# Optimization experiments

Hardware: AMD Instinct MI355X
Metric: run time of the kernel (lower is better)

## Reference

```python
import jax, jax.numpy as jnp
import numpy as np

N, E, ND, ED, NG = 100000, 1600000, 256, 32, 64
H1, H2 = 5, 1  # hard-coded hidden widths in the module
EPS = 1e-5


def setup_inputs() -> dict:
    key = jax.random.key(0)
    ks = jax.random.split(key, 32)

    def rn(k, shape, scale=0.05):
        return jax.random.normal(k, shape, dtype=jnp.float32) * scale

    inp = {
        "x": rn(ks[0], (N, ND), 1.0),
        "edge_attr": rn(ks[1], (E, ED), 1.0),
        "edge_index": jax.random.randint(ks[2], (2, E), 0, N, dtype=jnp.int32),
        "batch_idx": jnp.sort(jax.random.randint(ks[3], (N,), 0, NG, dtype=jnp.int32)),
        # conv1: ResGatedGraphConv(ND -> H1) with edge_dim=ED, root_weight, bias
        "Wk1": rn(ks[4], (ND, H1)), "bk1": jnp.zeros((H1,), jnp.float32),
        "Wq1": rn(ks[5], (ND, H1)), "bq1": jnp.zeros((H1,), jnp.float32),
        "Wv1": rn(ks[6], (ND, H1)), "bv1": jnp.zeros((H1,), jnp.float32),
        "We1": rn(ks[7], (ED, H1)), "be1": jnp.zeros((H1,), jnp.float32),
        "Ws1": rn(ks[8], (ND, H1)), "b1": jnp.zeros((H1,), jnp.float32),
        # GraphNorm(H1): weight=1, bias=0, mean_scale=1 at init
        "gw": jnp.ones((H1,), jnp.float32), "gb": jnp.zeros((H1,), jnp.float32),
        "gms": jnp.ones((H1,), jnp.float32),
        # conv2: ResGatedGraphConv(H1 -> H2)
        "Wk2": rn(ks[9], (H1, H2)), "bk2": jnp.zeros((H2,), jnp.float32),
        "Wq2": rn(ks[10], (H1, H2)), "bq2": jnp.zeros((H2,), jnp.float32),
        "Wv2": rn(ks[11], (H1, H2)), "bv2": jnp.zeros((H2,), jnp.float32),
        "We2": rn(ks[12], (ED, H2)), "be2": jnp.zeros((H2,), jnp.float32),
        "Ws2": rn(ks[13], (H1, H2)), "b2": jnp.zeros((H2,), jnp.float32),
    }
    return inp


def _res_gated_conv(x, src, dst, eatt, Wk, bk, Wq, bq, Wv, bv, We, be, Ws, b):
    # PyG ResGatedGraphConv: msg = sigmoid(k_i + q_j) * v_j with edge_attr
    # projection added to k, q, v; aggr='add'; plus root skip and bias.
    k = x @ Wk + bk            # [N,H]
    q = x @ Wq + bq            # [N,H]
    v = x @ Wv + bv            # [N,H]
    e = eatt @ We + be         # [E,H]
    gate = jax.nn.sigmoid(k[dst] + q[src] + 2.0 * e)  # (k_i+e)+(q_j+e)
    msg = gate * (v[src] + e)                          # [E,H]
    agg = jax.ops.segment_sum(msg, dst, num_segments=x.shape[0])
    return agg + x @ Ws + b


def _graph_norm(x, batch, w, b, ms):
    ones = jnp.ones((x.shape[0], 1), x.dtype)
    cnt = jnp.maximum(jax.ops.segment_sum(ones, batch, num_segments=NG), 1.0)
    mean = jax.ops.segment_sum(x, batch, num_segments=NG) / cnt
    out = x - mean[batch] * ms
    var = jax.ops.segment_sum(out * out, batch, num_segments=NG) / cnt
    inv_std = jax.lax.rsqrt(var + EPS)
    return w * out * inv_std[batch] + b


def reference(x, edge_attr, edge_index, batch_idx,
              Wk1, bk1, Wq1, bq1, Wv1, bv1, We1, be1, Ws1, b1,
              gw, gb, gms,
              Wk2, bk2, Wq2, bq2, Wv2, bv2, We2, be2, Ws2, b2):
    src, dst = edge_index[0], edge_index[1]
    h = _res_gated_conv(x, src, dst, edge_attr, Wk1, bk1, Wq1, bq1, Wv1, bv1,
                        We1, be1, Ws1, b1)
    h = _graph_norm(h, batch_idx, gw, gb, gms)
    h = jax.nn.relu(h)
    h = _res_gated_conv(h, src, dst, edge_attr, Wk2, bk2, Wq2, bq2, Wv2, bv2,
                        We2, be2, Ws2, b2)
    return jax.nn.sigmoid(h)
```

## Files before the change

### kernel.cpp

```cpp
#include <hip/hip_runtime.h>
#include <math.h>

#define ND 256
#define ED 32
#define H1 5
#define NG 64
#define SCAN_TILE 1024

__device__ __forceinline__ float sigf(float z) {
    return 1.0f / (1.0f + __expf(-z));
}

__global__ void node_proj1(const float* __restrict__ x,
                           const float* __restrict__ Wk, const float* __restrict__ bk,
                           const float* __restrict__ Wq, const float* __restrict__ bq,
                           const float* __restrict__ Wv, const float* __restrict__ bv,
                           const float* __restrict__ Ws, const float* __restrict__ br,
                           float* __restrict__ kqv, float* __restrict__ h, int N)
{
    int n = blockIdx.x * blockDim.x + threadIdx.x;
    if (n >= N) return;

    float acc[20];
#pragma unroll
    for (int c = 0; c < H1; c++) {
        acc[c]      = bk[c];
        acc[5 + c]  = bq[c];
        acc[10 + c] = bv[c];
        acc[15 + c] = br[c];
    }

    const float4* X4 = (const float4*)(x + (size_t)n * ND);
#pragma unroll 2
    for (int j4 = 0; j4 < ND / 4; j4++) {
        float4 xv = X4[j4];
        float xr[4] = {xv.x, xv.y, xv.z, xv.w};
#pragma unroll
        for (int r = 0; r < 4; r++) {
            int j = j4 * 4 + r;
#pragma unroll
            for (int c = 0; c < H1; c++) {
                acc[c]      += xr[r] * Wk[j * H1 + c];
                acc[5 + c]  += xr[r] * Wq[j * H1 + c];
                acc[10 + c] += xr[r] * Wv[j * H1 + c];
                acc[15 + c] += xr[r] * Ws[j * H1 + c];
            }
        }
    }

    float* row = kqv + (size_t)n * 16;
#pragma unroll
    for (int c = 0; c < H1; c++) {
        row[c]      = acc[5 + c];
        row[5 + c]  = acc[10 + c];
        row[10 + c] = acc[c];
    }
    row[15] = 0.0f;
#pragma unroll
    for (int c = 0; c < H1; c++) h[(size_t)n * H1 + c] = acc[15 + c];
}

__global__ void hist_dst(const int* __restrict__ ei, int* __restrict__ cnt, int E)
{
    int e = blockIdx.x * blockDim.x + threadIdx.x;
    if (e < E) atomicAdd(&cnt[ei[E + e]], 1);
}

__global__ void scan_part(const int* __restrict__ cnt, int* __restrict__ bsum, int N)
{
    int t = threadIdx.x;
    int base = blockIdx.x * SCAN_TILE + t * 4;
    int s = 0;
    if (base + 3 < N) {
        int4 v = *(const int4*)(cnt + base);
        s = v.x + v.y + v.z + v.w;
    } else {
        for (int i = 0; i < 4; i++) if (base + i < N) s += cnt[base + i];
    }
#pragma unroll
    for (int off = 32; off >= 1; off >>= 1) s += __shfl_xor(s, off);
    __shared__ int wsum[4];
    if ((t & 63) == 0) wsum[t >> 6] = s;
    __syncthreads();
    if (t == 0) bsum[blockIdx.x] = wsum[0] + wsum[1] + wsum[2] + wsum[3];
}

__global__ void scan_blocksums(int* __restrict__ bsum, int nb)
{
    __shared__ int a[1024], b[1024];
    int t = threadIdx.x;
    int v = (t < nb) ? bsum[t] : 0;
    a[t] = v;
    __syncthreads();
    int* in = a; int* out = b;
    for (int off = 1; off < 1024; off <<= 1) {
        out[t] = in[t] + ((t >= off) ? in[t - off] : 0);
        __syncthreads();
        int* tmp = in; in = out; out = tmp;
    }
    if (t < nb) bsum[t] = in[t] - v;
}

__global__ void scan_final(const int* __restrict__ cnt, const int* __restrict__ bsum,
                           int* __restrict__ offs, int* __restrict__ cursor, int N, int E)
{
    int t = threadIdx.x;
    int lane = t & 63;
    int wave = t >> 6;
    int base = blockIdx.x * SCAN_TILE + t * 4;

    int v0 = 0, v1 = 0, v2 = 0, v3 = 0;
    if (base + 3 < N) {
        int4 v = *(const int4*)(cnt + base);
        v0 = v.x; v1 = v.y; v2 = v.z; v3 = v.w;
    } else {
        if (base + 0 < N) v0 = cnt[base + 0];
        if (base + 1 < N) v1 = cnt[base + 1];
        if (base + 2 < N) v2 = cnt[base + 2];
        if (base + 3 < N) v3 = cnt[base + 3];
    }
    int s = v0 + v1 + v2 + v3;

    int inc = s;
#pragma unroll
    for (int off = 1; off < 64; off <<= 1) {
        int u = __shfl_up(inc, off);
        if (lane >= off) inc += u;
    }

    __shared__ int wtot[4];
    if (lane == 63) wtot[wave] = inc;
    __syncthreads();
    int woff = 0;
#pragma unroll
    for (int w = 0; w < 4; w++) woff += (w < wave) ? wtot[w] : 0;

    int excl = bsum[blockIdx.x] + woff + (inc - s);

    if (base < N) {
        int p0 = excl, p1 = p0 + v0, p2 = p1 + v1, p3 = p2 + v2;
        if (base + 3 < N) {
            *(int4*)(offs + base)   = make_int4(p0, p1, p2, p3);
            *(int4*)(cursor + base) = make_int4(p0, p1, p2, p3);
        } else {
            if (base + 0 < N) { offs[base + 0] = p0; cursor[base + 0] = p0; }
            if (base + 1 < N) { offs[base + 1] = p1; cursor[base + 1] = p1; }
            if (base + 2 < N) { offs[base + 2] = p2; cursor[base + 2] = p2; }
            if (base + 3 < N) { offs[base + 3] = p3; cursor[base + 3] = p3; }
        }
    }
    if (blockIdx.x == 0 && t == 0) offs[N] = E;
}

__global__ void edge_scatter(const float* __restrict__ ea, const int* __restrict__ ei,
                             const float* __restrict__ We1, const float* __restrict__ be1,
                             const float* __restrict__ We2, const float* __restrict__ be2,
                             int* __restrict__ cursor, float* __restrict__ sorted, int E)
{
    __shared__ float lds[256 * 33];
    int t = threadIdx.x;
    int base = blockIdx.x * 256;
    int nEdge = min(256, E - base);

    const float4* g = (const float4*)(ea + (size_t)base * ED);
    for (int k = t; k < nEdge * 8; k += 256) {
        float4 v = g[k];
        int f = k * 4;
        int r = f >> 5, c = f & 31;
        float* p = &lds[r * 33 + c];
        p[0] = v.x; p[1] = v.y; p[2] = v.z; p[3] = v.w;
    }
    __syncthreads();

    int e = base + t;
    if (e >= E) return;

    float acc0 = be1[0], acc1 = be1[1], acc2 = be1[2], acc3 = be1[3], acc4 = be1[4];
    float acc5 = be2[0];
    const float* myrow = &lds[t * 33];
#pragma unroll
    for (int j = 0; j < ED; j++) {
        float a = myrow[j];
        acc0 += a * We1[j * H1 + 0];
        acc1 += a * We1[j * H1 + 1];
        acc2 += a * We1[j * H1 + 2];
        acc3 += a * We1[j * H1 + 3];
        acc4 += a * We1[j * H1 + 4];
        acc5 += a * We2[j];
    }

    int s = ei[e];
    int d = ei[E + e];
    int pos = atomicAdd(&cursor[d], 1);

    float4* rec = (float4*)(sorted + (size_t)pos * 8);
    rec[0] = make_float4(__int_as_float(s), acc0, acc1, acc2);
    rec[1] = make_float4(acc3, acc4, acc5, 0.0f);
}

__global__ void aggregate1(const float* __restrict__ sorted, const int* __restrict__ offs,
                           const float* __restrict__ kqv, float* __restrict__ h, int N)
{
    int t = threadIdx.x;
    int n = blockIdx.x * 16 + (t >> 4);
    int lane = t & 15;
    if (n >= N) return;

    int start = offs[n], end = offs[n + 1];

    const float4* row = (const float4*)(kqv + (size_t)n * 16);
    float4 kA = row[2];
    float4 kB = row[3];
    float kd0 = kA.z, kd1 = kA.w, kd2 = kB.x, kd3 = kB.y, kd4 = kB.z;

    float m0 = 0, m1 = 0, m2 = 0, m3 = 0, m4 = 0;
    for (int i = start + lane; i < end; i += 16) {
        const float4* rec = (const float4*)(sorted + (size_t)i * 8);
        float4 r0 = rec[0];
        float4 r1 = rec[1];
        int s = __float_as_int(r0.x);
        const float4* srow = (const float4*)(kqv + (size_t)s * 16);
        float4 q0 = srow[0];
        float4 q1 = srow[1];
        float4 q2 = srow[2];
        m0 += sigf(kd0 + q0.x + 2.0f * r0.y) * (q1.y + r0.y);
        m1 += sigf(kd1 + q0.y + 2.0f * r0.z) * (q1.z + r0.z);
        m2 += sigf(kd2 + q0.z + 2.0f * r0.w) * (q1.w + r0.w);
        m3 += sigf(kd3 + q0.w + 2.0f * r1.x) * (q2.x + r1.x);
        m4 += sigf(kd4 + q1.x + 2.0f * r1.y) * (q2.y + r1.y);
    }

#pragma unroll
    for (int off = 8; off >= 1; off >>= 1) {
        m0 += __shfl_xor(m0, off);
        m1 += __shfl_xor(m1, off);
        m2 += __shfl_xor(m2, off);
        m3 += __shfl_xor(m3, off);
        m4 += __shfl_xor(m4, off);
    }

    if (lane == 0) {
        size_t base = (size_t)n * H1;
        h[base + 0] += m0;
        h[base + 1] += m1;
        h[base + 2] += m2;
        h[base + 3] += m3;
        h[base + 4] += m4;
    }
}

__global__ void norm_reduce(const float* __restrict__ h, const int* __restrict__ B,
                            const float* __restrict__ gw, const float* __restrict__ gb,
                            const float* __restrict__ gms,
                            float* __restrict__ scale, float* __restrict__ shift, int N)
{
    int g = blockIdx.x;

    int lo = 0, hi = N;
    while (lo < hi) { int mid = (lo + hi) >> 1; if (B[mid] < g) lo = mid + 1; else hi = mid; }
    int start = lo;
    hi = N;
    while (lo < hi) { int mid = (lo + hi) >> 1; if (B[mid] < g + 1) lo = mid + 1; else hi = mid; }
    int end = lo;

    float sum[H1] = {0, 0, 0, 0, 0};
    float sq[H1]  = {0, 0, 0, 0, 0};
    for (int i = start + threadIdx.x; i < end; i += blockDim.x) {
#pragma unroll
        for (int c = 0; c < H1; c++) {
            float v = h[(size_t)i * H1 + c];
            sum[c] += v;
            sq[c]  += v * v;
        }
    }

#pragma unroll
    for (int off = 32; off >= 1; off >>= 1) {
#pragma unroll
        for (int c = 0; c < H1; c++) {
            sum[c] += __shfl_xor(sum[c], off);
            sq[c]  += __shfl_xor(sq[c], off);
        }
    }

    __shared__ float ls[4][2 * H1];
    int wave = threadIdx.x >> 6;
    int lane = threadIdx.x & 63;
    if (lane == 0) {
#pragma unroll
        for (int c = 0; c < H1; c++) { ls[wave][c] = sum[c]; ls[wave][H1 + c] = sq[c]; }
    }
    __syncthreads();

    if (threadIdx.x == 0) {
        float cnt = fmaxf((float)(end - start), 1.0f);
#pragma unroll
        for (int c = 0; c < H1; c++) {
            float s0 = ls[0][c] + ls[1][c] + ls[2][c] + ls[3][c];
            float q0 = ls[0][H1 + c] + ls[1][H1 + c] + ls[2][H1 + c] + ls[3][H1 + c];
            float mean = s0 / cnt;
            float ms   = gms[c];
            float var  = q0 / cnt - mean * mean * ms * (2.0f - ms);
            float inv  = rsqrtf(var + 1e-5f);
            float sc   = gw[c] * inv;
            scale[g * H1 + c] = sc;
            shift[g * H1 + c] = gb[c] - sc * mean * ms;
        }
    }
}

__global__ void norm_apply_proj2(const float* __restrict__ h, const int* __restrict__ B,
                                 const float* __restrict__ scale, const float* __restrict__ shift,
                                 const float* __restrict__ Wk2, const float* __restrict__ bk2,
                                 const float* __restrict__ Wq2, const float* __restrict__ bq2,
                                 const float* __restrict__ Wv2, const float* __restrict__ bv2,
                                 const float* __restrict__ Ws2, const float* __restrict__ b2,
                                 float4* __restrict__ kqv2, float* __restrict__ root2, int N)
{
    int n = blockIdx.x * blockDim.x + threadIdx.x;
    if (n >= N) return;

    int g = B[n];
    float k2 = bk2[0], q2 = bq2[0], v2 = bv2[0], s2 = b2[0];
#pragma unroll
    for (int c = 0; c < H1; c++) {
        float hn = scale[g * H1 + c] * h[(size_t)n * H1 + c] + shift[g * H1 + c];
        hn = fmaxf(hn, 0.0f);
        k2 += hn * Wk2[c];
        q2 += hn * Wq2[c];
        v2 += hn * Wv2[c];
        s2 += hn * Ws2[c];
    }
    kqv2[n]  = make_float4(k2, q2, v2, 0.0f);
    root2[n] = s2;
}

__global__ void aggregate2(const float* __restrict__ sorted, const int* __restrict__ offs,
                           const float4* __restrict__ kqv2, const float* __restrict__ root2,
                           float* __restrict__ out, int N)
{
    int t = threadIdx.x;
    int n = blockIdx.x * 16 + (t >> 4);
    int lane = t & 15;
    if (n >= N) return;

    int start = offs[n], end = offs[n + 1];
    float kd = kqv2[n].x;

    float m = 0;
    for (int i = start + lane; i < end; i += 16) {
        const float4* rec = (const float4*)(sorted + (size_t)i * 8);
        float4 r0 = rec[0];
        float4 r1 = rec[1];
        int s = __float_as_int(r0.x);
        float e2 = r1.z;
        float4 sv = kqv2[s];
        m += sigf(kd + sv.y + 2.0f * e2) * (sv.z + e2);
    }

#pragma unroll
    for (int off = 8; off >= 1; off >>= 1) m += __shfl_xor(m, off);

    if (lane == 0) out[n] = sigf(root2[n] + m);
}

extern "C" void kernel_launch(void* const* d_in, const int* in_sizes, int n_in,
                              void* d_out, int out_size, void* d_ws, size_t ws_size,
                              hipStream_t stream)
{
    const float* x   = (const float*)d_in[0];
    const float* ea  = (const float*)d_in[1];
    const int*   ei  = (const int*)d_in[2];
    const int*   B   = (const int*)d_in[3];
    const float* Wk1 = (const float*)d_in[4];
    const float* bk1 = (const float*)d_in[5];
    const float* Wq1 = (const float*)d_in[6];
    const float* bq1 = (const float*)d_in[7];
    const float* Wv1 = (const float*)d_in[8];
    const float* bv1 = (const float*)d_in[9];
    const float* We1 = (const float*)d_in[10];
    const float* be1 = (const float*)d_in[11];
    const float* Ws1 = (const float*)d_in[12];
    const float* b1  = (const float*)d_in[13];
    const float* gw  = (const float*)d_in[14];
    const float* gb  = (const float*)d_in[15];
    const float* gms = (const float*)d_in[16];
    const float* Wk2 = (const float*)d_in[17];
    const float* bk2 = (const float*)d_in[18];
    const float* Wq2 = (const float*)d_in[19];
    const float* bq2 = (const float*)d_in[20];
    const float* Wv2 = (const float*)d_in[21];
    const float* bv2 = (const float*)d_in[22];
    const float* We2 = (const float*)d_in[23];
    const float* be2 = (const float*)d_in[24];
    const float* Ws2 = (const float*)d_in[25];
    const float* b2  = (const float*)d_in[26];

    const int N = in_sizes[0] / ND;
    const int E = in_sizes[1] / ED;
    const int nb = (N + SCAN_TILE - 1) / SCAN_TILE;

    float* ws      = (float*)d_ws;
    float* kqv     = ws;
    float* h       = kqv + (size_t)N * 16;
    float* sorted  = h + (size_t)N * H1;
    int*   cnt     = (int*)(sorted + (size_t)E * 8);
    int*   offs    = cnt + N;
    int*   cursor  = offs + N + 4;
    int*   bsum    = cursor + N;
    float* scale   = (float*)(bsum + 1024);
    float* shift   = scale + NG * H1;
    float* kqv2f   = shift + NG * H1 + 2;
    kqv2f = (float*)(bsum + 1024) + 640;
    float* root2   = kqv2f + (size_t)N * 4;
    float4* kqv2   = (float4*)kqv2f;

    dim3 blk(256);
    dim3 gN((N + 255) / 256);
    dim3 gE((E + 255) / 256);
    dim3 gAgg((N + 15) / 16);

    hipMemsetAsync(cnt, 0, (size_t)N * sizeof(int), stream);

    hist_dst<<<gE, blk, 0, stream>>>(ei, cnt, E);
    node_proj1<<<gN, blk, 0, stream>>>(x, Wk1, bk1, Wq1, bq1, Wv1, bv1, Ws1, b1,
                                       kqv, h, N);
    scan_part<<<nb, 256, 0, stream>>>(cnt, bsum, N);
    scan_blocksums<<<1, 1024, 0, stream>>>(bsum, nb);
    scan_final<<<nb, 256, 0, stream>>>(cnt, bsum, offs, cursor, N, E);
    edge_scatter<<<gE, blk, 0, stream>>>(ea, ei, We1, be1, We2, be2, cursor, sorted, E);
    aggregate1<<<gAgg, blk, 0, stream>>>(sorted, offs, kqv, h, N);
    norm_reduce<<<NG, blk, 0, stream>>>(h, B, gw, gb, gms, scale, shift, N);
    norm_apply_proj2<<<gN, blk, 0, stream>>>(h, B, scale, shift,
                                             Wk2, bk2, Wq2, bq2, Wv2, bv2, Ws2, b2,
                                             kqv2, root2, N);
    aggregate2<<<gAgg, blk, 0, stream>>>(sorted, offs, kqv2, root2, (float*)d_out, N);
}
```

Before: 654.0 us.

## Replace CSR sort-and-gather aggregation with per-edge atomic scatter

Removes the histogram, three-pass scan and counting-sort scatter that built a destination-sorted edge list. Each edge now computes its projection, message and gate directly and atomically adds into the destination node's accumulators for both conv layers. A small per-edge buffer keeps the layer-2 edge projection. This drops several kernel launches and the sorted record traffic, but it makes float atomics contend on destinations and makes the summation order nondeterministic. Loading edge_attr per thread as float4 rows also gives up the coalesced LDS staging the old scatter kernel used.

```diff
diff --git a/kernel.cpp b/kernel.cpp
--- a/kernel.cpp
+++ b/kernel.cpp
@@ -5,7 +5,6 @@
 #define ED 32
 #define H1 5
 #define NG 64
-#define SCAN_TILE 1024
 
 __device__ __forceinline__ float sigf(float z) {
     return 1.0f / (1.0f + __expf(-z));
@@ -60,193 +59,63 @@
     for (int c = 0; c < H1; c++) h[(size_t)n * H1 + c] = acc[15 + c];
 }
 
-__global__ void hist_dst(const int* __restrict__ ei, int* __restrict__ cnt, int E)
+__global__ void edge1(const float* __restrict__ ea, const int* __restrict__ ei,
+                      const float* __restrict__ We1, const float* __restrict__ be1,
+                      const float* __restrict__ We2, const float* __restrict__ be2,
+                      const float* __restrict__ kqv, float* __restrict__ h,
+                      float* __restrict__ e2buf, int E)
 {
     int e = blockIdx.x * blockDim.x + threadIdx.x;
-    if (e < E) atomicAdd(&cnt[ei[E + e]], 1);
-}
-
-__global__ void scan_part(const int* __restrict__ cnt, int* __restrict__ bsum, int N)
-{
-    int t = threadIdx.x;
-    int base = blockIdx.x * SCAN_TILE + t * 4;
-    int s = 0;
-    if (base + 3 < N) {
-        int4 v = *(const int4*)(cnt + base);
-        s = v.x + v.y + v.z + v.w;
-    } else {
-        for (int i = 0; i < 4; i++) if (base + i < N) s += cnt[base + i];
-    }
-#pragma unroll
-    for (int off = 32; off >= 1; off >>= 1) s += __shfl_xor(s, off);
-    __shared__ int wsum[4];
-    if ((t & 63) == 0) wsum[t >> 6] = s;
-    __syncthreads();
-    if (t == 0) bsum[blockIdx.x] = wsum[0] + wsum[1] + wsum[2] + wsum[3];
-}
-
-__global__ void scan_blocksums(int* __restrict__ bsum, int nb)
-{
-    __shared__ int a[1024], b[1024];
-    int t = threadIdx.x;
-    int v = (t < nb) ? bsum[t] : 0;
-    a[t] = v;
-    __syncthreads();
-    int* in = a; int* out = b;
-    for (int off = 1; off < 1024; off <<= 1) {
-        out[t] = in[t] + ((t >= off) ? in[t - off] : 0);
-        __syncthreads();
-        int* tmp = in; in = out; out = tmp;
-    }
-    if (t < nb) bsum[t] = in[t] - v;
-}
-
-__global__ void scan_final(const int* __restrict__ cnt, const int* __restrict__ bsum,
-                           int* __restrict__ offs, int* __restrict__ cursor, int N, int E)
-{
-    int t = threadIdx.x;
-    int lane = t & 63;
-    int wave = t >> 6;
-    int base = blockIdx.x * SCAN_TILE + t * 4;
-
-    int v0 = 0, v1 = 0, v2 = 0, v3 = 0;
-    if (base + 3 < N) {
-        int4 v = *(const int4*)(cnt + base);
-        v0 = v.x; v1 = v.y; v2 = v.z; v3 = v.w;
-    } else {
-        if (base + 0 < N) v0 = cnt[base + 0];
-        if (base + 1 < N) v1 = cnt[base + 1];
-        if (base + 2 < N) v2 = cnt[base + 2];
-        if (base + 3 < N) v3 = cnt[base + 3];
-    }
-    int s = v0 + v1 + v2 + v3;
-
-    int inc = s;
-#pragma unroll
-    for (int off = 1; off < 64; off <<= 1) {
-        int u = __shfl_up(inc, off);
-        if (lane >= off) inc += u;
-    }
-
-    __shared__ int wtot[4];
-    if (lane == 63) wtot[wave] = inc;
-    __syncthreads();
-    int woff = 0;
-#pragma unroll
-    for (int w = 0; w < 4; w++) woff += (w < wave) ? wtot[w] : 0;
-
-    int excl = bsum[blockIdx.x] + woff + (inc - s);
-
-    if (base < N) {
-        int p0 = excl, p1 = p0 + v0, p2 = p1 + v1, p3 = p2 + v2;
-        if (base + 3 < N) {
-            *(int4*)(offs + base)   = make_int4(p0, p1, p2, p3);
-            *(int4*)(cursor + base) = make_int4(p0, p1, p2, p3);
-        } else {
-            if (base + 0 < N) { offs[base + 0] = p0; cursor[base + 0] = p0; }
-            if (base + 1 < N) { offs[base + 1] = p1; cursor[base + 1] = p1; }
-            if (base + 2 < N) { offs[base + 2] = p2; cursor[base + 2] = p2; }
-            if (base + 3 < N) { offs[base + 3] = p3; cursor[base + 3] = p3; }
-        }
-    }
-    if (blockIdx.x == 0 && t == 0) offs[N] = E;
-}
-
-__global__ void edge_scatter(const float* __restrict__ ea, const int* __restrict__ ei,
-                             const float* __restrict__ We1, const float* __restrict__ be1,
-                             const float* __restrict__ We2, const float* __restrict__ be2,
-                             int* __restrict__ cursor, float* __restrict__ sorted, int E)
-{
-    __shared__ float lds[256 * 33];
-    int t = threadIdx.x;
-    int base = blockIdx.x * 256;
-    int nEdge = min(256, E - base);
-
-    const float4* g = (const float4*)(ea + (size_t)base * ED);
-    for (int k = t; k < nEdge * 8; k += 256) {
-        float4 v = g[k];
-        int f = k * 4;
-        int r = f >> 5, c = f & 31;
-        float* p = &lds[r * 33 + c];
-        p[0] = v.x; p[1] = v.y; p[2] = v.z; p[3] = v.w;
-    }
-    __syncthreads();
-
-    int e = base + t;
     if (e >= E) return;
 
-    float acc0 = be1[0], acc1 = be1[1], acc2 = be1[2], acc3 = be1[3], acc4 = be1[4];
-    float acc5 = be2[0];
-    const float* myrow = &lds[t * 33];
-#pragma unroll
-    for (int j = 0; j < ED; j++) {
-        float a = myrow[j];
-        acc0 += a * We1[j * H1 + 0];
-        acc1 += a * We1[j * H1 + 1];
-        acc2 += a * We1[j * H1 + 2];
-        acc3 += a * We1[j * H1 + 3];
-        acc4 += a * We1[j * H1 + 4];
-        acc5 += a * We2[j];
-    }
+    const float4* A4 = (const float4*)(ea + (size_t)e * ED);
+    float4 r[8];
+#pragma unroll
+    for (int j = 0; j < 8; j++) r[j] = A4[j];
 
     int s = ei[e];
     int d = ei[E + e];
-    int pos = atomicAdd(&cursor[d], 1);
-
-    float4* rec = (float4*)(sorted + (size_t)pos * 8);
-    rec[0] = make_float4(__int_as_float(s), acc0, acc1, acc2);
-    rec[1] = make_float4(acc3, acc4, acc5, 0.0f);
-}
-
-__global__ void aggregate1(const float* __restrict__ sorted, const int* __restrict__ offs,
-                           const float* __restrict__ kqv, float* __restrict__ h, int N)
-{
-    int t = threadIdx.x;
-    int n = blockIdx.x * 16 + (t >> 4);
-    int lane = t & 15;
-    if (n >= N) return;
-
-    int start = offs[n], end = offs[n + 1];
-
-    const float4* row = (const float4*)(kqv + (size_t)n * 16);
-    float4 kA = row[2];
-    float4 kB = row[3];
-    float kd0 = kA.z, kd1 = kA.w, kd2 = kB.x, kd3 = kB.y, kd4 = kB.z;
-
-    float m0 = 0, m1 = 0, m2 = 0, m3 = 0, m4 = 0;
-    for (int i = start + lane; i < end; i += 16) {
-        const float4* rec = (const float4*)(sorted + (size_t)i * 8);
-        float4 r0 = rec[0];
-        float4 r1 = rec[1];
-        int s = __float_as_int(r0.x);
-        const float4* srow = (const float4*)(kqv + (size_t)s * 16);
-        float4 q0 = srow[0];
-        float4 q1 = srow[1];
-        float4 q2 = srow[2];
-        m0 += sigf(kd0 + q0.x + 2.0f * r0.y) * (q1.y + r0.y);
-        m1 += sigf(kd1 + q0.y + 2.0f * r0.z) * (q1.z + r0.z);
-        m2 += sigf(kd2 + q0.z + 2.0f * r0.w) * (q1.w + r0.w);
-        m3 += sigf(kd3 + q0.w + 2.0f * r1.x) * (q2.x + r1.x);
-        m4 += sigf(kd4 + q1.x + 2.0f * r1.y) * (q2.y + r1.y);
-    }
-
-#pragma unroll
-    for (int off = 8; off >= 1; off >>= 1) {
-        m0 += __shfl_xor(m0, off);
-        m1 += __shfl_xor(m1, off);
-        m2 += __shfl_xor(m2, off);
-        m3 += __shfl_xor(m3, off);
-        m4 += __shfl_xor(m4, off);
-    }
-
-    if (lane == 0) {
-        size_t base = (size_t)n * H1;
-        h[base + 0] += m0;
-        h[base + 1] += m1;
-        h[base + 2] += m2;
-        h[base + 3] += m3;
-        h[base + 4] += m4;
-    }
+
+    float e10 = be1[0], e11 = be1[1], e12 = be1[2], e13 = be1[3], e14 = be1[4];
+    float e2  = be2[0];
+#pragma unroll
+    for (int j4 = 0; j4 < 8; j4++) {
+        float av[4] = {r[j4].x, r[j4].y, r[j4].z, r[j4].w};
+#pragma unroll
+        for (int t = 0; t < 4; t++) {
+            int j = j4 * 4 + t;
+            float a = av[t];
+            e10 += a * We1[j * H1 + 0];
+            e11 += a * We1[j * H1 + 1];
+            e12 += a * We1[j * H1 + 2];
+            e13 += a * We1[j * H1 + 3];
+            e14 += a * We1[j * H1 + 4];
+            e2  += a * We2[j];
+        }
+    }
+
+    const float4* srow = (const float4*)(kqv + (size_t)s * 16);
+    float4 q0 = srow[0];
+    float4 q1 = srow[1];
+    float4 q2 = srow[2];
+    const float4* drow = (const float4*)(kqv + (size_t)d * 16);
+    float4 kA = drow[2];
+    float4 kB = drow[3];
+
+    float m0 = sigf(kA.z + q0.x + 2.0f * e10) * (q1.y + e10);
+    float m1 = sigf(kA.w + q0.y + 2.0f * e11) * (q1.z + e11);
+    float m2 = sigf(kB.x + q0.z + 2.0f * e12) * (q1.w + e12);
+    float m3 = sigf(kB.y + q0.w + 2.0f * e13) * (q2.x + e13);
+    float m4 = sigf(kB.z + q1.x + 2.0f * e14) * (q2.y + e14);
+
+    float* hd = h + (size_t)d * H1;
+    atomicAdd(hd + 0, m0);
+    atomicAdd(hd + 1, m1);
+    atomicAdd(hd + 2, m2);
+    atomicAdd(hd + 3, m3);
+    atomicAdd(hd + 4, m4);
+
+    e2buf[e] = e2;
 }
 
 __global__ void norm_reduce(const float* __restrict__ h, const int* __restrict__ B,
@@ -335,33 +204,26 @@
     root2[n] = s2;
 }
 
-__global__ void aggregate2(const float* __restrict__ sorted, const int* __restrict__ offs,
-                           const float4* __restrict__ kqv2, const float* __restrict__ root2,
-                           float* __restrict__ out, int N)
-{
-    int t = threadIdx.x;
-    int n = blockIdx.x * 16 + (t >> 4);
-    int lane = t & 15;
-    if (n >= N) return;
-
-    int start = offs[n], end = offs[n + 1];
-    float kd = kqv2[n].x;
-
-    float m = 0;
-    for (int i = start + lane; i < end; i += 16) {
-        const float4* rec = (const float4*)(sorted + (size_t)i * 8);
-        float4 r0 = rec[0];
-        float4 r1 = rec[1];
-        int s = __float_as_int(r0.x);
-        float e2 = r1.z;
-        float4 sv = kqv2[s];
-        m += sigf(kd + sv.y + 2.0f * e2) * (sv.z + e2);
-    }
-
-#pragma unroll
-    for (int off = 8; off >= 1; off >>= 1) m += __shfl_xor(m, off);
-
-    if (lane == 0) out[n] = sigf(root2[n] + m);
+__global__ void edge2(const int* __restrict__ ei, const float* __restrict__ e2buf,
+                      const float4* __restrict__ kqv2, float* __restrict__ mbuf, int E)
+{
+    int e = blockIdx.x * blockDim.x + threadIdx.x;
+    if (e >= E) return;
+
+    int s = ei[e];
+    int d = ei[E + e];
+    float e2 = e2buf[e];
+    float4 sv = kqv2[s];
+    float kd = kqv2[d].x;
+    float m = sigf(kd + sv.y + 2.0f * e2) * (sv.z + e2);
+    atomicAdd(&mbuf[d], m);
+}
+
+__global__ void finalize(const float* __restrict__ root2, const float* __restrict__ mbuf,
+                         float* __restrict__ out, int N)
+{
+    int n = blockIdx.x * blockDim.x + threadIdx.x;
+    if (n < N) out[n] = sigf(root2[n] + mbuf[n]);
 }
 
 extern "C" void kernel_launch(void* const* d_in, const int* in_sizes, int n_in,
@@ -398,41 +260,31 @@
 
     const int N = in_sizes[0] / ND;
     const int E = in_sizes[1] / ED;
-    const int nb = (N + SCAN_TILE - 1) / SCAN_TILE;
-
-    float* ws      = (float*)d_ws;
-    float* kqv     = ws;
-    float* h       = kqv + (size_t)N * 16;
-    float* sorted  = h + (size_t)N * H1;
-    int*   cnt     = (int*)(sorted + (size_t)E * 8);
-    int*   offs    = cnt + N;
-    int*   cursor  = offs + N + 4;
-    int*   bsum    = cursor + N;
-    float* scale   = (float*)(bsum + 1024);
-    float* shift   = scale + NG * H1;
-    float* kqv2f   = shift + NG * H1 + 2;
-    kqv2f = (float*)(bsum + 1024) + 640;
-    float* root2   = kqv2f + (size_t)N * 4;
-    float4* kqv2   = (float4*)kqv2f;
+
+    float* ws     = (float*)d_ws;
+    float* kqv    = ws;
+    float* h      = kqv + (size_t)N * 16;
+    float* e2buf  = h + (size_t)N * H1;
+    float* scale  = e2buf + (size_t)E;
+    float* shift  = scale + NG * H1;
+    float* kqv2f  = shift + NG * H1;
+    float* root2  = kqv2f + (size_t)N * 4;
+    float* mbuf   = root2 + (size_t)N;
+    float4* kqv2  = (float4*)kqv2f;
 
     dim3 blk(256);
     dim3 gN((N + 255) / 256);
     dim3 gE((E + 255) / 256);
-    dim3 gAgg((N + 15) / 16);
-
-    hipMemsetAsync(cnt, 0, (size_t)N * sizeof(int), stream);
-
-    hist_dst<<<gE, blk, 0, stream>>>(ei, cnt, E);
+
+    hipMemsetAsync(mbuf, 0, (size_t)N * sizeof(float), stream);
+
     node_proj1<<<gN, blk, 0, stream>>>(x, Wk1, bk1, Wq1, bq1, Wv1, bv1, Ws1, b1,
                                        kqv, h, N);
-    scan_part<<<nb, 256, 0, stream>>>(cnt, bsum, N);
-    scan_blocksums<<<1, 1024, 0, stream>>>(bsum, nb);
-    scan_final<<<nb, 256, 0, stream>>>(cnt, bsum, offs, cursor, N, E);
-    edge_scatter<<<gE, blk, 0, stream>>>(ea, ei, We1, be1, We2, be2, cursor, sorted, E);
-    aggregate1<<<gAgg, blk, 0, stream>>>(sorted, offs, kqv, h, N);
+    edge1<<<gE, blk, 0, stream>>>(ea, ei, We1, be1, We2, be2, kqv, h, e2buf, E);
     norm_reduce<<<NG, blk, 0, stream>>>(h, B, gw, gb, gms, scale, shift, N);
     norm_apply_proj2<<<gN, blk, 0, stream>>>(h, B, scale, shift,
                                              Wk2, bk2, Wq2, bq2, Wv2, bv2, Ws2, b2,
                                              kqv2, root2, N);
-    aggregate2<<<gAgg, blk, 0, stream>>>(sorted, offs, kqv2, root2, (float*)d_out, N);
-}
+    edge2<<<gE, blk, 0, stream>>>(ei, e2buf, kqv2, mbuf, E);
+    finalize<<<gN, blk, 0, stream>>>(root2, mbuf, (float*)d_out, N);
+}
```

After: 917.3 us. 1.4x slower.

## Compute layer-1 edge messages in edge order and aggregate through a permutation index

Applied to the files above, without the earlier changes.

The edge kernel now reads the k/q/v rows of source and destination and computes the full layer-1 message per edge, writing it coherently at the edge's own index. A permutation array maps CSR slots to edge ids. aggregate1 then only sums precomputed messages via the permutation, and aggregate2 gathers the edge term and the source index through it. The scattered 32-byte record writes become coalesced writes, and the gather work moves from aggregation into the edge kernel. In exchange the aggregation reads become indirect, edge_msg reads the edge attributes per thread without the LDS staging it used before, and aggregate2 now does an extra indirect read of edge_index.

```diff
diff --git a/kernel.cpp b/kernel.cpp
--- a/kernel.cpp
+++ b/kernel.cpp
@@ -152,54 +152,66 @@
     if (blockIdx.x == 0 && t == 0) offs[N] = E;
 }
 
-__global__ void edge_scatter(const float* __restrict__ ea, const int* __restrict__ ei,
-                             const float* __restrict__ We1, const float* __restrict__ be1,
-                             const float* __restrict__ We2, const float* __restrict__ be2,
-                             int* __restrict__ cursor, float* __restrict__ sorted, int E)
-{
-    __shared__ float lds[256 * 33];
-    int t = threadIdx.x;
-    int base = blockIdx.x * 256;
-    int nEdge = min(256, E - base);
-
-    const float4* g = (const float4*)(ea + (size_t)base * ED);
-    for (int k = t; k < nEdge * 8; k += 256) {
-        float4 v = g[k];
-        int f = k * 4;
-        int r = f >> 5, c = f & 31;
-        float* p = &lds[r * 33 + c];
-        p[0] = v.x; p[1] = v.y; p[2] = v.z; p[3] = v.w;
-    }
-    __syncthreads();
-
-    int e = base + t;
+__global__ void edge_msg(const float* __restrict__ ea, const int* __restrict__ ei,
+                         const float* __restrict__ We1, const float* __restrict__ be1,
+                         const float* __restrict__ We2, const float* __restrict__ be2,
+                         const float* __restrict__ kqv, int* __restrict__ cursor,
+                         float4* __restrict__ recA, float2* __restrict__ recB,
+                         int* __restrict__ perm, int E)
+{
+    int e = blockIdx.x * blockDim.x + threadIdx.x;
     if (e >= E) return;
 
-    float acc0 = be1[0], acc1 = be1[1], acc2 = be1[2], acc3 = be1[3], acc4 = be1[4];
-    float acc5 = be2[0];
-    const float* myrow = &lds[t * 33];
-#pragma unroll
-    for (int j = 0; j < ED; j++) {
-        float a = myrow[j];
-        acc0 += a * We1[j * H1 + 0];
-        acc1 += a * We1[j * H1 + 1];
-        acc2 += a * We1[j * H1 + 2];
-        acc3 += a * We1[j * H1 + 3];
-        acc4 += a * We1[j * H1 + 4];
-        acc5 += a * We2[j];
-    }
+    const float4* A4 = (const float4*)(ea + (size_t)e * ED);
+    float4 r[8];
+#pragma unroll
+    for (int j = 0; j < 8; j++) r[j] = A4[j];
 
     int s = ei[e];
     int d = ei[E + e];
     int pos = atomicAdd(&cursor[d], 1);
 
-    float4* rec = (float4*)(sorted + (size_t)pos * 8);
-    rec[0] = make_float4(__int_as_float(s), acc0, acc1, acc2);
-    rec[1] = make_float4(acc3, acc4, acc5, 0.0f);
-}
-
-__global__ void aggregate1(const float* __restrict__ sorted, const int* __restrict__ offs,
-                           const float* __restrict__ kqv, float* __restrict__ h, int N)
+    const float4* srow = (const float4*)(kqv + (size_t)s * 16);
+    float4 q0 = srow[0];
+    float4 q1 = srow[1];
+    float4 q2 = srow[2];
+    const float4* drow = (const float4*)(kqv + (size_t)d * 16);
+    float4 kA = drow[2];
+    float4 kB = drow[3];
+
+    float e10 = be1[0], e11 = be1[1], e12 = be1[2], e13 = be1[3], e14 = be1[4];
+    float e2  = be2[0];
+#pragma unroll
+    for (int j4 = 0; j4 < 8; j4++) {
+        float av[4] = {r[j4].x, r[j4].y, r[j4].z, r[j4].w};
+#pragma unroll
+        for (int t = 0; t < 4; t++) {
+            int j = j4 * 4 + t;
+            float a = av[t];
+            e10 += a * We1[j * H1 + 0];
+            e11 += a * We1[j * H1 + 1];
+            e12 += a * We1[j * H1 + 2];
+            e13 += a * We1[j * H1 + 3];
+            e14 += a * We1[j * H1 + 4];
+            e2  += a * We2[j];
+        }
+    }
+
+    float m0 = sigf(kA.z + q0.x + 2.0f * e10) * (q1.y + e10);
+    float m1 = sigf(kA.w + q0.y + 2.0f * e11) * (q1.z + e11);
+    float m2 = sigf(kB.x + q0.z + 2.0f * e12) * (q1.w + e12);
+    float m3 = sigf(kB.y + q0.w + 2.0f * e13) * (q2.x + e13);
+    float m4 = sigf(kB.z + q1.x + 2.0f * e14) * (q2.y + e14);
+
+    recA[e] = make_float4(m0, m1, m2, m3);
+    recB[e] = make_float2(m4, e2);
+
+    perm[pos] = e;
+}
+
+__global__ void aggregate1(const int* __restrict__ perm, const int* __restrict__ offs,
+                           const float4* __restrict__ recA, const float2* __restrict__ recB,
+                           float* __restrict__ h, int N)
 {
     int t = threadIdx.x;
     int n = blockIdx.x * 16 + (t >> 4);
@@ -208,26 +220,12 @@
 
     int start = offs[n], end = offs[n + 1];
 
-    const float4* row = (const float4*)(kqv + (size_t)n * 16);
-    float4 kA = row[2];
-    float4 kB = row[3];
-    float kd0 = kA.z, kd1 = kA.w, kd2 = kB.x, kd3 = kB.y, kd4 = kB.z;
-
     float m0 = 0, m1 = 0, m2 = 0, m3 = 0, m4 = 0;
     for (int i = start + lane; i < end; i += 16) {
-        const float4* rec = (const float4*)(sorted + (size_t)i * 8);
-        float4 r0 = rec[0];
-        float4 r1 = rec[1];
-        int s = __float_as_int(r0.x);
-        const float4* srow = (const float4*)(kqv + (size_t)s * 16);
-        float4 q0 = srow[0];
-        float4 q1 = srow[1];
-        float4 q2 = srow[2];
-        m0 += sigf(kd0 + q0.x + 2.0f * r0.y) * (q1.y + r0.y);
-        m1 += sigf(kd1 + q0.y + 2.0f * r0.z) * (q1.z + r0.z);
-        m2 += sigf(kd2 + q0.z + 2.0f * r0.w) * (q1.w + r0.w);
-        m3 += sigf(kd3 + q0.w + 2.0f * r1.x) * (q2.x + r1.x);
-        m4 += sigf(kd4 + q1.x + 2.0f * r1.y) * (q2.y + r1.y);
+        int e = perm[i];
+        float4 a = recA[e];
+        float2 b = recB[e];
+        m0 += a.x; m1 += a.y; m2 += a.z; m3 += a.w; m4 += b.x;
     }
 
 #pragma unroll
@@ -335,7 +333,8 @@
     root2[n] = s2;
 }
 
-__global__ void aggregate2(const float* __restrict__ sorted, const int* __restrict__ offs,
+__global__ void aggregate2(const int* __restrict__ perm, const int* __restrict__ offs,
+                           const float2* __restrict__ recB, const int* __restrict__ ei,
                            const float4* __restrict__ kqv2, const float* __restrict__ root2,
                            float* __restrict__ out, int N)
 {
@@ -349,11 +348,10 @@
 
     float m = 0;
     for (int i = start + lane; i < end; i += 16) {
-        const float4* rec = (const float4*)(sorted + (size_t)i * 8);
-        float4 r0 = rec[0];
-        float4 r1 = rec[1];
-        int s = __float_as_int(r0.x);
-        float e2 = r1.z;
+        int e = perm[i];
+        float2 b = recB[e];
+        float e2 = b.y;
+        int s = ei[e];
         float4 sv = kqv2[s];
         m += sigf(kd + sv.y + 2.0f * e2) * (sv.z + e2);
     }
@@ -400,20 +398,23 @@
     const int E = in_sizes[1] / ED;
     const int nb = (N + SCAN_TILE - 1) / SCAN_TILE;
 
-    float* ws      = (float*)d_ws;
-    float* kqv     = ws;
-    float* h       = kqv + (size_t)N * 16;
-    float* sorted  = h + (size_t)N * H1;
-    int*   cnt     = (int*)(sorted + (size_t)E * 8);
-    int*   offs    = cnt + N;
-    int*   cursor  = offs + N + 4;
-    int*   bsum    = cursor + N;
-    float* scale   = (float*)(bsum + 1024);
-    float* shift   = scale + NG * H1;
-    float* kqv2f   = shift + NG * H1 + 2;
-    kqv2f = (float*)(bsum + 1024) + 640;
-    float* root2   = kqv2f + (size_t)N * 4;
-    float4* kqv2   = (float4*)kqv2f;
+    float* ws     = (float*)d_ws;
+    float* kqv    = ws;
+    float* h      = kqv + (size_t)N * 16;
+    float* recAf  = h + (size_t)N * H1;
+    float* recBf  = recAf + (size_t)E * 4;
+    int*   perm   = (int*)(recBf + (size_t)E * 2);
+    int*   cnt    = perm + (size_t)E;
+    int*   offs   = cnt + N;
+    int*   cursor = offs + N + 4;
+    int*   bsum   = cursor + N;
+    float* scale  = (float*)(bsum + 1024);
+    float* shift  = scale + NG * H1;
+    float* kqv2f  = shift + NG * H1;
+    float* root2  = kqv2f + (size_t)N * 4;
+    float4* kqv2  = (float4*)kqv2f;
+    float4* recA  = (float4*)recAf;
+    float2* recB  = (float2*)recBf;
 
     dim3 blk(256);
     dim3 gN((N + 255) / 256);
@@ -428,11 +429,13 @@
     scan_part<<<nb, 256, 0, stream>>>(cnt, bsum, N);
     scan_blocksums<<<1, 1024, 0, stream>>>(bsum, nb);
     scan_final<<<nb, 256, 0, stream>>>(cnt, bsum, offs, cursor, N, E);
-    edge_scatter<<<gE, blk, 0, stream>>>(ea, ei, We1, be1, We2, be2, cursor, sorted, E);
-    aggregate1<<<gAgg, blk, 0, stream>>>(sorted, offs, kqv, h, N);
+    edge_msg<<<gE, blk, 0, stream>>>(ea, ei, We1, be1, We2, be2, kqv, cursor,
+                                     recA, recB, perm, E);
+    aggregate1<<<gAgg, blk, 0, stream>>>(perm, offs, recA, recB, h, N);
     norm_reduce<<<NG, blk, 0, stream>>>(h, B, gw, gb, gms, scale, shift, N);
     norm_apply_proj2<<<gN, blk, 0, stream>>>(h, B, scale, shift,
                                              Wk2, bk2, Wq2, bq2, Wv2, bv2, Ws2, b2,
                                              kqv2, root2, N);
-    aggregate2<<<gAgg, blk, 0, stream>>>(sorted, offs, kqv2, root2, (float*)d_out, N);
-}
+    aggregate2<<<gAgg, blk, 0, stream>>>(perm, offs, recB, ei, kqv2, root2,
+                                         (float*)d_out, N);
+}
```

Result: slower. 758.2 us (+15.9%).
